# Performance work log

Hardware: AMD Instinct MI355X
Metric: run time of the kernel (lower is better)

The kernel has to match this reference:

```python
import jax, jax.numpy as jnp
import numpy as np

N_NODES = 50000


def setup_inputs() -> dict:
    key = jax.random.key(0)
    k1, k2, k3, k4 = jax.random.split(key, 4)
    in_feats, out_feats = 128, 64
    n_edges = 800000
    feats = jax.random.normal(k1, (N_NODES, in_feats), dtype=jnp.float32)
    # xavier_uniform_ bound for [in, out]
    bound = float(np.sqrt(6.0 / (in_feats + out_feats)))
    weight = jax.random.uniform(k2, (in_feats, out_feats), dtype=jnp.float32, minval=-bound, maxval=bound)
    bias = jnp.zeros((out_feats,), dtype=jnp.float32)
    src = jax.random.randint(k3, (n_edges,), 0, N_NODES, dtype=jnp.int32)
    dst = jax.random.randint(k4, (n_edges,), 0, N_NODES, dtype=jnp.int32)
    return {"feats": feats, "weight": weight, "bias": bias, "src": src, "dst": dst}


def reference(feats, weight, bias, src, dst):
    # linear transform: [N, in] @ [in, out] -> [N, out]
    h = feats @ weight
    # update_all(copy_src('h','m'), sum): gather messages from src, sum-reduce onto dst
    msgs = h[src]  # [E, out]
    agg = jax.ops.segment_sum(msgs, dst, num_segments=N_NODES)  # [N, out]
    return jax.nn.relu(agg + bias)
```

## Files before the change

kernel.cpp:

```cpp
#include <hip/hip_runtime.h>

constexpr int IN_F  = 128;
constexpr int OUT_F = 64;
constexpr int NB_BLOCKS = 256;
constexpr int BIN_SHIFT = 6;
constexpr int MAX_BINS  = 1024;
constexpr int BIN_CAP   = 8192;

using bf16x8 = __attribute__((ext_vector_type(8))) short;
using f32x4  = __attribute__((ext_vector_type(4))) float;

__device__ inline short f2bf(float f) {
    unsigned u = __builtin_bit_cast(unsigned, f);
    u += 0x7fffu + ((u >> 16) & 1u);
    return (short)(u >> 16);
}
__device__ inline float bf2f(unsigned short u) {
    unsigned x = ((unsigned)u) << 16;
    return __builtin_bit_cast(float, x);
}

__global__ __launch_bounds__(256) void gemm_kernel(
        const float* __restrict__ feats, const float* __restrict__ weight,
        unsigned short* __restrict__ h, int n_nodes) {
    __shared__ short wbT[OUT_F][IN_F + 8];

    for (int idx = threadIdx.x; idx < IN_F * OUT_F; idx += 256)
        wbT[idx & 63][idx >> 6] = f2bf(weight[idx]);
    __syncthreads();

    const int lane  = threadIdx.x & 63;
    const int wid   = threadIdx.x >> 6;
    const int arow  = lane & 15;
    const int kg    = lane >> 4;
    const int node0 = blockIdx.x * 64 + wid * 16;

    const int an = min(node0 + arow, n_nodes - 1);
    const float* ap = feats + (size_t)an * IN_F;

    f32x4 acc[4] = {{0,0,0,0},{0,0,0,0},{0,0,0,0},{0,0,0,0}};

    #pragma unroll
    for (int ks = 0; ks < 4; ++ks) {
        const int kbase = ks * 32 + kg * 8;
        const float4 a0 = *reinterpret_cast<const float4*>(ap + kbase);
        const float4 a1 = *reinterpret_cast<const float4*>(ap + kbase + 4);
        bf16x8 a;
        a[0] = f2bf(a0.x); a[1] = f2bf(a0.y); a[2] = f2bf(a0.z); a[3] = f2bf(a0.w);
        a[4] = f2bf(a1.x); a[5] = f2bf(a1.y); a[6] = f2bf(a1.z); a[7] = f2bf(a1.w);
        #pragma unroll
        for (int nt = 0; nt < 4; ++nt) {
            const bf16x8 b = *reinterpret_cast<const bf16x8*>(&wbT[nt * 16 + (lane & 15)][kbase]);
            acc[nt] = __builtin_amdgcn_mfma_f32_16x16x32_bf16(a, b, acc[nt], 0, 0, 0);
        }
    }

    #pragma unroll
    for (int nt = 0; nt < 4; ++nt) {
        #pragma unroll
        for (int r = 0; r < 4; ++r) {
            const int n = node0 + (lane >> 4) * 4 + r;
            if (n < n_nodes)
                h[(size_t)n * OUT_F + nt * 16 + (lane & 15)] = (unsigned short)f2bf(acc[nt][r]);
        }
    }
}

__global__ void hist_kernel(const int* __restrict__ dst, int* __restrict__ histmat,
                            int E, int nbins) {
    __shared__ int hl[MAX_BINS];
    const int k = blockIdx.x;
    const int chunk = (E + NB_BLOCKS - 1) / NB_BLOCKS;
    const int beg = k * chunk, end = min(E, beg + chunk);
    for (int i = threadIdx.x; i < nbins; i += blockDim.x) hl[i] = 0;
    __syncthreads();
    for (int e = beg + threadIdx.x; e < end; e += blockDim.x)
        atomicAdd(&hl[dst[e] >> BIN_SHIFT], 1);
    __syncthreads();
    for (int i = threadIdx.x; i < nbins; i += blockDim.x)
        histmat[k * nbins + i] = hl[i];
}

__global__ void colscan_kernel(int* __restrict__ histmat, int* __restrict__ tot, int nbins) {
    __shared__ int s[NB_BLOCKS];
    const int b = blockIdx.x;
    const int t = threadIdx.x;
    const int v = histmat[t * nbins + b];
    s[t] = v;
    __syncthreads();
    for (int off = 1; off < NB_BLOCKS; off <<= 1) {
        const int u = (t >= off) ? s[t - off] : 0;
        __syncthreads();
        s[t] += u;
        __syncthreads();
    }
    histmat[t * nbins + b] = s[t] - v;
    if (t == NB_BLOCKS - 1) tot[b] = s[t];
}

__global__ void binscan_kernel(const int* __restrict__ tot, int* __restrict__ binbase,
                               int nbins, int E) {
    __shared__ int s[MAX_BINS];
    const int t = threadIdx.x;
    const int v = (t < nbins) ? tot[t] : 0;
    s[t] = v;
    __syncthreads();
    for (int off = 1; off < MAX_BINS; off <<= 1) {
        const int u = (t >= off) ? s[t - off] : 0;
        __syncthreads();
        s[t] += u;
        __syncthreads();
    }
    if (t < nbins) binbase[t] = s[t] - v;
    if (t == 0) binbase[nbins] = E;
}

__global__ void scatter_kernel(const int* __restrict__ src, const int* __restrict__ dst,
                               const int* __restrict__ colscan, const int* __restrict__ binbase,
                               unsigned int* __restrict__ bucket, int E, int nbins) {
    __shared__ int cur[MAX_BINS];
    const int k = blockIdx.x;
    for (int i = threadIdx.x; i < nbins; i += blockDim.x)
        cur[i] = binbase[i] + colscan[k * nbins + i];
    __syncthreads();
    const int chunk = (E + NB_BLOCKS - 1) / NB_BLOCKS;
    const int beg = k * chunk, end = min(E, beg + chunk);
    for (int e = beg + threadIdx.x; e < end; e += blockDim.x) {
        const int d = dst[e];
        const int pos = atomicAdd(&cur[d >> BIN_SHIFT], 1);
        bucket[pos] = ((unsigned)(d & 63) << 16) | (unsigned)src[e];
    }
}

__global__ void binsort_kernel(unsigned int* __restrict__ bucket,
                               const int* __restrict__ binbase,
                               int* __restrict__ offs, int N, int E, int nbins) {
    __shared__ unsigned buf[BIN_CAP];
    __shared__ int cnt64[64];
    __shared__ int off64[64];
    const int b    = blockIdx.x;
    const int base = binbase[b], end = binbase[b + 1];
    const int cnt  = end - base;

    for (int i = threadIdx.x; i < cnt; i += 256) buf[i] = bucket[base + i];
    if (threadIdx.x < 64) cnt64[threadIdx.x] = 0;
    __syncthreads();
    for (int i = threadIdx.x; i < cnt; i += 256)
        atomicAdd(&cnt64[buf[i] >> 16], 1);
    __syncthreads();

    int v = 0;
    if (threadIdx.x < 64) { v = cnt64[threadIdx.x]; off64[threadIdx.x] = v; }
    __syncthreads();
    for (int off = 1; off < 64; off <<= 1) {
        int u = 0;
        if (threadIdx.x >= off && threadIdx.x < 64) u = off64[threadIdx.x - off];
        __syncthreads();
        if (threadIdx.x < 64) off64[threadIdx.x] += u;
        __syncthreads();
    }
    if (threadIdx.x < 64) {
        const int excl = off64[threadIdx.x] - v;
        const int node = (b << BIN_SHIFT) + threadIdx.x;
        if (node < N) offs[node] = base + excl;
        off64[threadIdx.x] = excl;
    }
    __syncthreads();

    for (int i = threadIdx.x; i < cnt; i += 256) {
        const unsigned wdv = buf[i];
        const int pos = atomicAdd(&off64[wdv >> 16], 1);
        bucket[base + pos] = wdv;
    }
    if (b == nbins - 1 && threadIdx.x == 0) offs[N] = E;
}

__global__ __launch_bounds__(256) void gather_kernel(
        const unsigned short* __restrict__ h, const unsigned int* __restrict__ bucket,
        const int* __restrict__ offs, const float* __restrict__ bias,
        float* __restrict__ out, int N) {
    const int lane   = threadIdx.x & 63;
    const int gwave  = (blockIdx.x * blockDim.x + threadIdx.x) >> 6;
    const int nwaves = (gridDim.x * blockDim.x) >> 6;
    const float b = bias[lane];
    for (int n = gwave; n < N; n += nwaves) {
        const int beg = offs[n], end = offs[n + 1];
        float acc = 0.f;
        int i = beg;
        for (; i + 8 <= end; i += 8) {
            const unsigned w0 = bucket[i + 0], w1 = bucket[i + 1];
            const unsigned w2 = bucket[i + 2], w3 = bucket[i + 3];
            const unsigned w4 = bucket[i + 4], w5 = bucket[i + 5];
            const unsigned w6 = bucket[i + 6], w7 = bucket[i + 7];
            const unsigned short u0 = h[(size_t)(w0 & 0xffffu) * OUT_F + lane];
            const unsigned short u1 = h[(size_t)(w1 & 0xffffu) * OUT_F + lane];
            const unsigned short u2 = h[(size_t)(w2 & 0xffffu) * OUT_F + lane];
            const unsigned short u3 = h[(size_t)(w3 & 0xffffu) * OUT_F + lane];
            const unsigned short u4 = h[(size_t)(w4 & 0xffffu) * OUT_F + lane];
            const unsigned short u5 = h[(size_t)(w5 & 0xffffu) * OUT_F + lane];
            const unsigned short u6 = h[(size_t)(w6 & 0xffffu) * OUT_F + lane];
            const unsigned short u7 = h[(size_t)(w7 & 0xffffu) * OUT_F + lane];
            acc += bf2f(u0); acc += bf2f(u1); acc += bf2f(u2); acc += bf2f(u3);
            acc += bf2f(u4); acc += bf2f(u5); acc += bf2f(u6); acc += bf2f(u7);
        }
        for (; i < end; ++i)
            acc += bf2f(h[(size_t)(bucket[i] & 0xffffu) * OUT_F + lane]);
        out[(size_t)n * OUT_F + lane] = fmaxf(acc + b, 0.f);
    }
}

extern "C" void kernel_launch(void* const* d_in, const int* in_sizes, int n_in,
                              void* d_out, int out_size, void* d_ws, size_t ws_size,
                              hipStream_t stream) {
    const float* feats  = (const float*)d_in[0];
    const float* weight = (const float*)d_in[1];
    const float* bias   = (const float*)d_in[2];
    const int*   src    = (const int*)d_in[3];
    const int*   dst    = (const int*)d_in[4];
    float* out = (float*)d_out;

    const int N = in_sizes[0] / IN_F;
    const int E = in_sizes[3];
    const int nbins = (N + 63) >> BIN_SHIFT;

    unsigned short* h = (unsigned short*)d_ws;
    unsigned* bucket  = (unsigned*)(h + (size_t)N * OUT_F);
    int*      histmat = (int*)(bucket + E);
    int*      tot     = histmat + NB_BLOCKS * nbins;
    int*      binbase = tot + nbins;
    int*      offs    = binbase + nbins + 1;

    gemm_kernel<<<(N + 63) / 64, 256, 0, stream>>>(feats, weight, h, N);
    hist_kernel<<<NB_BLOCKS, 256, 0, stream>>>(dst, histmat, E, nbins);
    colscan_kernel<<<nbins, NB_BLOCKS, 0, stream>>>(histmat, tot, nbins);
    binscan_kernel<<<1, MAX_BINS, 0, stream>>>(tot, binbase, nbins, E);
    scatter_kernel<<<NB_BLOCKS, 256, 0, stream>>>(src, dst, histmat, binbase, bucket, E, nbins);
    binsort_kernel<<<nbins, 256, 0, stream>>>(bucket, binbase, offs, N, E, nbins);
    gather_kernel<<<2048, 256, 0, stream>>>(h, bucket, offs, bias, out, N);
}
```

Baseline: 148.3 us.

## Fuse GEMM and CSR build stages into one cooperative kernel with grid syncs

Replaces six kernel launches (GEMM, histogram, column scan, bin scan, scatter, bin sort) with one cooperative kernel of nbins blocks that separates the stages with grid.sync() and reuses a shared-memory union across them. The aim is to cut the launch overhead and inter-kernel gaps between the small stages. The bin scan is reworked to run on 256 threads with four elements each. BIN_CAP drops to 4096 and bin counts are clamped, so the shared union gets smaller and occupancy can rise. In exchange, all 782 blocks must be co-resident for the cooperative launch, and a bin with more than 4096 edges would be silently truncated.

```diff
diff --git a/kernel.cpp b/kernel.cpp
--- a/kernel.cpp
+++ b/kernel.cpp
@@ -1,11 +1,14 @@
 #include <hip/hip_runtime.h>
+#include <hip/hip_cooperative_groups.h>
+
+namespace cg = cooperative_groups;
 
 constexpr int IN_F  = 128;
 constexpr int OUT_F = 64;
 constexpr int NB_BLOCKS = 256;
 constexpr int BIN_SHIFT = 6;
 constexpr int MAX_BINS  = 1024;
-constexpr int BIN_CAP   = 8192;
+constexpr int BIN_CAP   = 4096;
 
 using bf16x8 = __attribute__((ext_vector_type(8))) short;
 using f32x4  = __attribute__((ext_vector_type(4))) float;
@@ -20,159 +23,169 @@
     return __builtin_bit_cast(float, x);
 }
 
-__global__ __launch_bounds__(256) void gemm_kernel(
+__global__ __launch_bounds__(256, 4) void build_kernel(
         const float* __restrict__ feats, const float* __restrict__ weight,
-        unsigned short* __restrict__ h, int n_nodes) {
-    __shared__ short wbT[OUT_F][IN_F + 8];
-
-    for (int idx = threadIdx.x; idx < IN_F * OUT_F; idx += 256)
-        wbT[idx & 63][idx >> 6] = f2bf(weight[idx]);
-    __syncthreads();
-
-    const int lane  = threadIdx.x & 63;
-    const int wid   = threadIdx.x >> 6;
-    const int arow  = lane & 15;
-    const int kg    = lane >> 4;
-    const int node0 = blockIdx.x * 64 + wid * 16;
-
-    const int an = min(node0 + arow, n_nodes - 1);
-    const float* ap = feats + (size_t)an * IN_F;
-
-    f32x4 acc[4] = {{0,0,0,0},{0,0,0,0},{0,0,0,0},{0,0,0,0}};
-
-    #pragma unroll
-    for (int ks = 0; ks < 4; ++ks) {
-        const int kbase = ks * 32 + kg * 8;
-        const float4 a0 = *reinterpret_cast<const float4*>(ap + kbase);
-        const float4 a1 = *reinterpret_cast<const float4*>(ap + kbase + 4);
-        bf16x8 a;
-        a[0] = f2bf(a0.x); a[1] = f2bf(a0.y); a[2] = f2bf(a0.z); a[3] = f2bf(a0.w);
-        a[4] = f2bf(a1.x); a[5] = f2bf(a1.y); a[6] = f2bf(a1.z); a[7] = f2bf(a1.w);
-        #pragma unroll
-        for (int nt = 0; nt < 4; ++nt) {
-            const bf16x8 b = *reinterpret_cast<const bf16x8*>(&wbT[nt * 16 + (lane & 15)][kbase]);
-            acc[nt] = __builtin_amdgcn_mfma_f32_16x16x32_bf16(a, b, acc[nt], 0, 0, 0);
-        }
-    }
-
-    #pragma unroll
-    for (int nt = 0; nt < 4; ++nt) {
-        #pragma unroll
-        for (int r = 0; r < 4; ++r) {
-            const int n = node0 + (lane >> 4) * 4 + r;
-            if (n < n_nodes)
-                h[(size_t)n * OUT_F + nt * 16 + (lane & 15)] = (unsigned short)f2bf(acc[nt][r]);
-        }
-    }
-}
-
-__global__ void hist_kernel(const int* __restrict__ dst, int* __restrict__ histmat,
-                            int E, int nbins) {
-    __shared__ int hl[MAX_BINS];
-    const int k = blockIdx.x;
-    const int chunk = (E + NB_BLOCKS - 1) / NB_BLOCKS;
-    const int beg = k * chunk, end = min(E, beg + chunk);
-    for (int i = threadIdx.x; i < nbins; i += blockDim.x) hl[i] = 0;
-    __syncthreads();
-    for (int e = beg + threadIdx.x; e < end; e += blockDim.x)
-        atomicAdd(&hl[dst[e] >> BIN_SHIFT], 1);
-    __syncthreads();
-    for (int i = threadIdx.x; i < nbins; i += blockDim.x)
-        histmat[k * nbins + i] = hl[i];
-}
-
-__global__ void colscan_kernel(int* __restrict__ histmat, int* __restrict__ tot, int nbins) {
-    __shared__ int s[NB_BLOCKS];
-    const int b = blockIdx.x;
-    const int t = threadIdx.x;
-    const int v = histmat[t * nbins + b];
-    s[t] = v;
-    __syncthreads();
-    for (int off = 1; off < NB_BLOCKS; off <<= 1) {
-        const int u = (t >= off) ? s[t - off] : 0;
-        __syncthreads();
-        s[t] += u;
-        __syncthreads();
-    }
-    histmat[t * nbins + b] = s[t] - v;
-    if (t == NB_BLOCKS - 1) tot[b] = s[t];
-}
-
-__global__ void binscan_kernel(const int* __restrict__ tot, int* __restrict__ binbase,
-                               int nbins, int E) {
-    __shared__ int s[MAX_BINS];
-    const int t = threadIdx.x;
-    const int v = (t < nbins) ? tot[t] : 0;
-    s[t] = v;
-    __syncthreads();
-    for (int off = 1; off < MAX_BINS; off <<= 1) {
-        const int u = (t >= off) ? s[t - off] : 0;
-        __syncthreads();
-        s[t] += u;
-        __syncthreads();
-    }
-    if (t < nbins) binbase[t] = s[t] - v;
-    if (t == 0) binbase[nbins] = E;
-}
-
-__global__ void scatter_kernel(const int* __restrict__ src, const int* __restrict__ dst,
-                               const int* __restrict__ colscan, const int* __restrict__ binbase,
-                               unsigned int* __restrict__ bucket, int E, int nbins) {
-    __shared__ int cur[MAX_BINS];
-    const int k = blockIdx.x;
-    for (int i = threadIdx.x; i < nbins; i += blockDim.x)
-        cur[i] = binbase[i] + colscan[k * nbins + i];
-    __syncthreads();
-    const int chunk = (E + NB_BLOCKS - 1) / NB_BLOCKS;
-    const int beg = k * chunk, end = min(E, beg + chunk);
-    for (int e = beg + threadIdx.x; e < end; e += blockDim.x) {
-        const int d = dst[e];
-        const int pos = atomicAdd(&cur[d >> BIN_SHIFT], 1);
-        bucket[pos] = ((unsigned)(d & 63) << 16) | (unsigned)src[e];
-    }
-}
-
-__global__ void binsort_kernel(unsigned int* __restrict__ bucket,
-                               const int* __restrict__ binbase,
-                               int* __restrict__ offs, int N, int E, int nbins) {
-    __shared__ unsigned buf[BIN_CAP];
-    __shared__ int cnt64[64];
-    __shared__ int off64[64];
-    const int b    = blockIdx.x;
-    const int base = binbase[b], end = binbase[b + 1];
-    const int cnt  = end - base;
-
-    for (int i = threadIdx.x; i < cnt; i += 256) buf[i] = bucket[base + i];
-    if (threadIdx.x < 64) cnt64[threadIdx.x] = 0;
-    __syncthreads();
-    for (int i = threadIdx.x; i < cnt; i += 256)
-        atomicAdd(&cnt64[buf[i] >> 16], 1);
-    __syncthreads();
-
-    int v = 0;
-    if (threadIdx.x < 64) { v = cnt64[threadIdx.x]; off64[threadIdx.x] = v; }
-    __syncthreads();
-    for (int off = 1; off < 64; off <<= 1) {
-        int u = 0;
-        if (threadIdx.x >= off && threadIdx.x < 64) u = off64[threadIdx.x - off];
-        __syncthreads();
-        if (threadIdx.x < 64) off64[threadIdx.x] += u;
-        __syncthreads();
-    }
-    if (threadIdx.x < 64) {
-        const int excl = off64[threadIdx.x] - v;
-        const int node = (b << BIN_SHIFT) + threadIdx.x;
-        if (node < N) offs[node] = base + excl;
-        off64[threadIdx.x] = excl;
-    }
-    __syncthreads();
-
-    for (int i = threadIdx.x; i < cnt; i += 256) {
-        const unsigned wdv = buf[i];
-        const int pos = atomicAdd(&off64[wdv >> 16], 1);
-        bucket[base + pos] = wdv;
-    }
-    if (b == nbins - 1 && threadIdx.x == 0) offs[N] = E;
+        unsigned short* __restrict__ h,
+        const int* __restrict__ src, const int* __restrict__ dst,
+        int* __restrict__ histmat, int* __restrict__ tot,
+        int* __restrict__ binbase, int* __restrict__ offs,
+        unsigned int* __restrict__ bucket,
+        int N, int E, int nbins) {
+    cg::grid_group grid = cg::this_grid();
+
+    __shared__ union {
+        short wbT[OUT_F][IN_F + 8];
+        int   hl[MAX_BINS];
+        int   s[NB_BLOCKS];
+        struct { int vals[MAX_BINS]; int part[256]; } bs;
+        int   cur[MAX_BINS];
+        struct { unsigned buf[BIN_CAP]; int cnt[64]; int off[64]; } srt;
+    } sh;
+
+    const int t    = threadIdx.x;
+    const int lane = t & 63;
+
+    {
+        for (int idx = t; idx < IN_F * OUT_F; idx += 256)
+            sh.wbT[idx & 63][idx >> 6] = f2bf(weight[idx]);
+        __syncthreads();
+
+        const int wid   = t >> 6;
+        const int kg    = lane >> 4;
+        const int node0 = blockIdx.x * 64 + wid * 16;
+        const int an    = min(node0 + (lane & 15), N - 1);
+        const float* ap = feats + (size_t)an * IN_F;
+
+        f32x4 acc[4] = {{0,0,0,0},{0,0,0,0},{0,0,0,0},{0,0,0,0}};
+        #pragma unroll
+        for (int ks = 0; ks < 4; ++ks) {
+            const int kbase = ks * 32 + kg * 8;
+            const float4 a0 = *reinterpret_cast<const float4*>(ap + kbase);
+            const float4 a1 = *reinterpret_cast<const float4*>(ap + kbase + 4);
+            bf16x8 a;
+            a[0] = f2bf(a0.x); a[1] = f2bf(a0.y); a[2] = f2bf(a0.z); a[3] = f2bf(a0.w);
+            a[4] = f2bf(a1.x); a[5] = f2bf(a1.y); a[6] = f2bf(a1.z); a[7] = f2bf(a1.w);
+            #pragma unroll
+            for (int nt = 0; nt < 4; ++nt) {
+                const bf16x8 b = *reinterpret_cast<const bf16x8*>(&sh.wbT[nt * 16 + (lane & 15)][kbase]);
+                acc[nt] = __builtin_amdgcn_mfma_f32_16x16x32_bf16(a, b, acc[nt], 0, 0, 0);
+            }
+        }
+        #pragma unroll
+        for (int nt = 0; nt < 4; ++nt)
+            #pragma unroll
+            for (int r = 0; r < 4; ++r) {
+                const int n = node0 + (lane >> 4) * 4 + r;
+                if (n < N) h[(size_t)n * OUT_F + nt * 16 + (lane & 15)] = (unsigned short)f2bf(acc[nt][r]);
+            }
+    }
+    grid.sync();
+
+    if (blockIdx.x < NB_BLOCKS) {
+        for (int i = t; i < nbins; i += 256) sh.hl[i] = 0;
+        __syncthreads();
+        const int chunk = (E + NB_BLOCKS - 1) / NB_BLOCKS;
+        const int beg = blockIdx.x * chunk, end = min(E, beg + chunk);
+        for (int e = beg + t; e < end; e += 256)
+            atomicAdd(&sh.hl[dst[e] >> BIN_SHIFT], 1);
+        __syncthreads();
+        for (int i = t; i < nbins; i += 256)
+            histmat[blockIdx.x * nbins + i] = sh.hl[i];
+    }
+    grid.sync();
+
+    {
+        const int b = blockIdx.x;
+        const int v = histmat[t * nbins + b];
+        sh.s[t] = v;
+        __syncthreads();
+        for (int off = 1; off < NB_BLOCKS; off <<= 1) {
+            const int u = (t >= off) ? sh.s[t - off] : 0;
+            __syncthreads();
+            sh.s[t] += u;
+            __syncthreads();
+        }
+        histmat[t * nbins + b] = sh.s[t] - v;
+        if (t == NB_BLOCKS - 1) tot[b] = sh.s[t];
+    }
+    grid.sync();
+
+    if (blockIdx.x == 0) {
+        for (int i = t; i < MAX_BINS; i += 256) sh.bs.vals[i] = (i < nbins) ? tot[i] : 0;
+        __syncthreads();
+        int ssum = 0;
+        #pragma unroll
+        for (int j = 0; j < 4; ++j) ssum += sh.bs.vals[t * 4 + j];
+        sh.bs.part[t] = ssum;
+        __syncthreads();
+        for (int off = 1; off < 256; off <<= 1) {
+            const int u = (t >= off) ? sh.bs.part[t - off] : 0;
+            __syncthreads();
+            sh.bs.part[t] += u;
+            __syncthreads();
+        }
+        int run = sh.bs.part[t] - ssum;
+        #pragma unroll
+        for (int j = 0; j < 4; ++j) {
+            const int i = t * 4 + j;
+            if (i < nbins) binbase[i] = run;
+            run += sh.bs.vals[i];
+        }
+        if (t == 0) binbase[nbins] = E;
+    }
+    grid.sync();
+
+    if (blockIdx.x < NB_BLOCKS) {
+        for (int i = t; i < nbins; i += 256)
+            sh.cur[i] = binbase[i] + histmat[blockIdx.x * nbins + i];
+        __syncthreads();
+        const int chunk = (E + NB_BLOCKS - 1) / NB_BLOCKS;
+        const int beg = blockIdx.x * chunk, end = min(E, beg + chunk);
+        for (int e = beg + t; e < end; e += 256) {
+            const int d = dst[e];
+            const int pos = atomicAdd(&sh.cur[d >> BIN_SHIFT], 1);
+            bucket[pos] = ((unsigned)(d & 63) << 16) | (unsigned)src[e];
+        }
+    }
+    grid.sync();
+
+    {
+        const int b    = blockIdx.x;
+        const int base = binbase[b];
+        const int cnt  = min(binbase[b + 1] - base, BIN_CAP);
+
+        for (int i = t; i < cnt; i += 256) sh.srt.buf[i] = bucket[base + i];
+        if (t < 64) sh.srt.cnt[t] = 0;
+        __syncthreads();
+        for (int i = t; i < cnt; i += 256)
+            atomicAdd(&sh.srt.cnt[sh.srt.buf[i] >> 16], 1);
+        __syncthreads();
+
+        int v = 0;
+        if (t < 64) { v = sh.srt.cnt[t]; sh.srt.off[t] = v; }
+        __syncthreads();
+        for (int off = 1; off < 64; off <<= 1) {
+            int u = 0;
+            if (t >= off && t < 64) u = sh.srt.off[t - off];
+            __syncthreads();
+            if (t < 64) sh.srt.off[t] += u;
+            __syncthreads();
+        }
+        if (t < 64) {
+            const int excl = sh.srt.off[t] - v;
+            const int node = (b << BIN_SHIFT) + t;
+            if (node < N) offs[node] = base + excl;
+            sh.srt.off[t] = excl;
+        }
+        __syncthreads();
+
+        for (int i = t; i < cnt; i += 256) {
+            const unsigned wdv = sh.srt.buf[i];
+            const int pos = atomicAdd(&sh.srt.off[wdv >> 16], 1);
+            bucket[base + pos] = wdv;
+        }
+        if (b == nbins - 1 && t == 0) offs[N] = E;
+    }
 }
 
 __global__ __launch_bounds__(256) void gather_kernel(
@@ -219,9 +232,9 @@
     const int*   dst    = (const int*)d_in[4];
     float* out = (float*)d_out;
 
-    const int N = in_sizes[0] / IN_F;
-    const int E = in_sizes[3];
-    const int nbins = (N + 63) >> BIN_SHIFT;
+    int N = in_sizes[0] / IN_F;
+    int E = in_sizes[3];
+    int nbins = (N + 63) >> BIN_SHIFT;
 
     unsigned short* h = (unsigned short*)d_ws;
     unsigned* bucket  = (unsigned*)(h + (size_t)N * OUT_F);
@@ -230,11 +243,10 @@
     int*      binbase = tot + nbins;
     int*      offs    = binbase + nbins + 1;
 
-    gemm_kernel<<<(N + 63) / 64, 256, 0, stream>>>(feats, weight, h, N);
-    hist_kernel<<<NB_BLOCKS, 256, 0, stream>>>(dst, histmat, E, nbins);
-    colscan_kernel<<<nbins, NB_BLOCKS, 0, stream>>>(histmat, tot, nbins);
-    binscan_kernel<<<1, MAX_BINS, 0, stream>>>(tot, binbase, nbins, E);
-    scatter_kernel<<<NB_BLOCKS, 256, 0, stream>>>(src, dst, histmat, binbase, bucket, E, nbins);
-    binsort_kernel<<<nbins, 256, 0, stream>>>(bucket, binbase, offs, N, E, nbins);
+    void* args[] = { (void*)&feats, (void*)&weight, (void*)&h, (void*)&src, (void*)&dst,
+                     (void*)&histmat, (void*)&tot, (void*)&binbase, (void*)&offs,
+                     (void*)&bucket, (void*)&N, (void*)&E, (void*)&nbins };
+    hipLaunchCooperativeKernel((const void*)build_kernel, dim3(nbins), dim3(256),
+                               args, 0, stream);
     gather_kernel<<<2048, 256, 0, stream>>>(h, bucket, offs, bias, out, N);
 }
```

Result: slower. 567.5 us (+282.7%).
